# Kernel tuning notes

Measured on AMD Instinct MI355X. Metric: run time of the kernel, lower is better.

Reference implementation:

```python
import jax, jax.numpy as jnp
import numpy as np

HIDDEN = 2048
INTER = 768
N_EXPERTS = 64
TOP_K = 8
BATCH, SEQ = 2, 2048


def setup_inputs() -> dict:
    key = jax.random.key(0)
    k_x, k_g, k_gp, k_up, k_dp = jax.random.split(key, 5)
    s_in = 1.0 / np.sqrt(HIDDEN)   # lecun_normal fan_in scaling
    s_mid = 1.0 / np.sqrt(INTER)
    return {
        "x": jax.random.normal(k_x, (BATCH, SEQ, HIDDEN), dtype=jnp.float32),
        "gate_w": jax.random.normal(k_g, (HIDDEN, N_EXPERTS), dtype=jnp.float32) * s_in,
        "gate_proj": jax.random.normal(k_gp, (N_EXPERTS, HIDDEN, INTER), dtype=jnp.float32) * s_in,
        "up_proj": jax.random.normal(k_up, (N_EXPERTS, HIDDEN, INTER), dtype=jnp.float32) * s_in,
        "down_proj": jax.random.normal(k_dp, (N_EXPERTS, INTER, HIDDEN), dtype=jnp.float32) * s_mid,
    }


def reference(x, gate_w, gate_proj, up_proj, down_proj):
    H = x.shape[-1]
    E = gate_proj.shape[0]
    K = TOP_K

    x_flat = x.reshape(-1, H)                      # [T, H]
    router_logits = x_flat @ gate_w                # [T, E]

    routing_weights, selected_experts = jax.lax.top_k(router_logits, k=K)  # [T, K]
    routing_weights = jax.nn.softmax(routing_weights, axis=-1)

    sel_flat = jnp.ravel(selected_experts)         # [T*K]
    x_expanded = jnp.repeat(x_flat, K, axis=0)     # [T*K, H]

    sort_idx = jnp.argsort(sel_flat)
    unsort_idx = jnp.argsort(sort_idx)
    x_sorted = x_expanded[sort_idx]                # tokens grouped by expert
    group_sizes = jnp.bincount(sel_flat, length=E)

    gate_out = jax.lax.ragged_dot(x_sorted, gate_proj, group_sizes)  # [T*K, I]
    up_out = jax.lax.ragged_dot(x_sorted, up_proj, group_sizes)      # [T*K, I]
    activated = jax.nn.silu(gate_out) * up_out
    down_out = jax.lax.ragged_dot(activated, down_proj, group_sizes)  # [T*K, H]

    unsorted = down_out[unsort_idx].reshape(-1, K, H)  # [T, K, H]
    out = (unsorted * routing_weights[..., None]).sum(axis=1)
    return out.reshape(x.shape), router_logits
```

## Files before the change

kernel.cpp:

```cpp
#include <hip/hip_runtime.h>
#include <hip/hip_bf16.h>
#include <cstdint>

#define NTOK 4096
#define HID  2048
#define ITER 768
#define NEXP 64
#define TOPK 8
#define MAXT 320

typedef __attribute__((ext_vector_type(8))) short sh8;
typedef __attribute__((ext_vector_type(4))) float f32x4;

#define MFMA16 __builtin_amdgcn_mfma_f32_16x16x32_bf16

__device__ __forceinline__ uint16_t f2b(float f) {
  union { float f; uint32_t u; } v; v.f = f;
  uint32_t u = v.u;
  u += 0x7FFFu + ((u >> 16) & 1u);
  return (uint16_t)(u >> 16);
}

__device__ __forceinline__ float b2f_lo(uint32_t w) {
  union { uint32_t u; float f; } v; v.u = w << 16; return v.f;
}
__device__ __forceinline__ float b2f_hi(uint32_t w) {
  union { uint32_t u; float f; } v; v.u = w & 0xffff0000u; return v.f;
}

__device__ __forceinline__ uint32_t cvtpk(float lo, float hi) {
  float2 f2; f2.x = lo; f2.y = hi;
  __hip_bfloat162 h = __float22bfloat162_rn(f2);
  union { __hip_bfloat162 h; uint32_t u; } v; v.h = h;
  return v.u;
}

__device__ __forceinline__ void gl2lds16(const void* g, void* l) {
  __builtin_amdgcn_global_load_lds(
      (const __attribute__((address_space(1))) uint32_t*)g,
      (__attribute__((address_space(3))) uint32_t*)l, 16, 0, 0);
}

__device__ __forceinline__ int xcd_unswizzle(int s, int na) {
  int q = na >> 3, r = na & 7, x = s & 7, i = s >> 3;
  return (x < r ? x * (q + 1) : r * (q + 1) + (x - r) * q) + i;
}

__global__ void zero_kernel(int* __restrict__ cc) {
  cc[threadIdx.x] = 0;
}

__global__ __launch_bounds__(256) void xcast_kernel(const float* __restrict__ x,
                                                    uint16_t* __restrict__ xb) {
  size_t i = ((size_t)blockIdx.x * 256 + threadIdx.x) * 8;
  float4 a = *(const float4*)(x + i);
  float4 b = *(const float4*)(x + i + 4);
  uint4 o;
  o.x = (uint32_t)f2b(a.x) | ((uint32_t)f2b(a.y) << 16);
  o.y = (uint32_t)f2b(a.z) | ((uint32_t)f2b(a.w) << 16);
  o.z = (uint32_t)f2b(b.x) | ((uint32_t)f2b(b.y) << 16);
  o.w = (uint32_t)f2b(b.z) | ((uint32_t)f2b(b.w) << 16);
  *(uint4*)(xb + i) = o;
}

__global__ __launch_bounds__(256) void router_kernel(
    const float* __restrict__ x, const float* __restrict__ gate_w,
    float* __restrict__ logits, int* __restrict__ topk_id,
    float* __restrict__ topk_w, int* __restrict__ counts)
{
  int lane = threadIdx.x & 63;
  int wv   = threadIdx.x >> 6;
  int t    = blockIdx.x * 4 + wv;
  const float* xr = x + (size_t)t * HID;
  float acc = 0.f;
  #pragma unroll 4
  for (int h = 0; h < HID; h += 4) {
    float4 xv = *(const float4*)(xr + h);
    acc += xv.x * gate_w[(h + 0) * NEXP + lane];
    acc += xv.y * gate_w[(h + 1) * NEXP + lane];
    acc += xv.z * gate_w[(h + 2) * NEXP + lane];
    acc += xv.w * gate_w[(h + 3) * NEXP + lane];
  }
  logits[(size_t)t * NEXP + lane] = acc;

  float v = acc;
  float topv[TOPK]; int topi[TOPK];
  #pragma unroll
  for (int k = 0; k < TOPK; ++k) {
    float bv = v; int bi = lane;
    #pragma unroll
    for (int off = 32; off > 0; off >>= 1) {
      float ov = __shfl_xor(bv, off);
      int   oi = __shfl_xor(bi, off);
      if (ov > bv || (ov == bv && oi < bi)) { bv = ov; bi = oi; }
    }
    topv[k] = bv; topi[k] = bi;
    if (lane == bi) v = -3.0e38f;
  }
  float m = topv[0], s = 0.f, w[TOPK];
  #pragma unroll
  for (int k = 0; k < TOPK; ++k) { w[k] = __expf(topv[k] - m); s += w[k]; }
  float inv = 1.f / s;
  if (lane < TOPK) {
    topk_id[t * TOPK + lane] = topi[lane];
    topk_w[t * TOPK + lane]  = w[lane] * inv;
    atomicAdd(&counts[topi[lane]], 1);
  }
}

__global__ void offsets_kernel(const int* __restrict__ counts, int* __restrict__ offsets,
                               int* __restrict__ tiles, int* __restrict__ tilecount) {
  if (threadIdx.x == 0) {
    int s = 0, nt = 0;
    for (int e = 0; e < NEXP; ++e) {
      offsets[e] = s;
      int c = counts[e];
      for (int rb = 0; rb * 128 < c; ++rb) tiles[nt++] = (e << 16) | rb;
      s += c;
    }
    offsets[NEXP] = s;
    tilecount[0] = nt;
  }
}

__global__ __launch_bounds__(256) void scatter_kernel(
    const int* __restrict__ topk_id,
    const int* __restrict__ offsets, int* __restrict__ cursor,
    int* __restrict__ pair_tok, int* __restrict__ inv)
{
  int p = blockIdx.x * 256 + threadIdx.x;
  int e = topk_id[p];
  int pos = offsets[e] + atomicAdd(&cursor[e], 1);
  pair_tok[pos] = p;
  inv[p] = pos;
}

__global__ __launch_bounds__(256, 2) void gateup_kernel(
    const uint16_t* __restrict__ xb,
    const float* __restrict__ gate_proj,
    const float* __restrict__ up_proj,
    const int* __restrict__ pair_tok,
    const int* __restrict__ offsets,
    const int* __restrict__ tiles,
    const int* __restrict__ tilecount,
    uint16_t* __restrict__ act)
{
  const int nt = tilecount[0];
  const int na = nt * 12;
  if (blockIdx.x >= na) return;
  const int L  = xcd_unswizzle(blockIdx.x, na);
  const int ti = L % nt, nc = L / nt;
  const int te = tiles[ti];
  const int e = te >> 16, row0 = (te & 0xffff) * 128;
  const int start = offsets[e];
  const int count = offsets[e + 1] - start;
  const int nvalid = min(128, count - row0);

  __shared__ __align__(16) uint16_t aT[128 * 64];
  __shared__ __align__(16) uint16_t bT[128 * 64];
  __shared__ int s_tok[128];

  const int t = threadIdx.x, l = t & 63, w = t >> 6;
  if (t < 128)
    s_tok[t] = (t < nvalid) ? (pair_tok[start + row0 + t] >> 3) : 0;
  __syncthreads();

  const int sub = l >> 3;
  const int xk  = ((l & 7) ^ sub) << 3;
  const uint16_t* srcA[4]; char* dstA[4];
  #pragma unroll
  for (int q = 0; q < 4; ++q) {
    int rl = (w * 4 + q) * 8 + sub;
    srcA[q] = xb + (size_t)s_tok[rl] * HID + xk;
    dstA[q] = (char*)aT + (w * 4 + q) * 1024;
  }

  const int brow = t & 127;
  const int kk0  = (t >> 7) * 32;
  const int rcomb  = nc * 128 + brow;
  const int n_orig = ((rcomb >> 5) << 4) + (rcomb & 15);
  const int is_up  = (rcomb >> 4) & 1;
  const float* wsrc = (is_up ? up_proj : gate_proj)
                    + (size_t)e * HID * ITER + n_orig;
  uint16_t* bwr[4];
  #pragma unroll
  for (int s = 0; s < 4; ++s) {
    int kb = (kk0 * 2 + 16 * s) ^ ((brow & 7) << 4);
    bwr[s] = (uint16_t*)((char*)bT + brow * 128 + kb);
  }

  const int wr = w >> 1, wc = w & 1, lr = l & 15, hi = l >> 4;
  const int xorv = (lr & 7) << 4;

  f32x4 acc[4][4];
  #pragma unroll
  for (int mi = 0; mi < 4; ++mi)
    #pragma unroll
    for (int ni = 0; ni < 4; ++ni)
      acc[mi][ni] = (f32x4){0.f, 0.f, 0.f, 0.f};

  for (int kc = 0; kc < 32; ++kc) {
    __syncthreads();
    float va[32];
    const float* wp = wsrc + (size_t)(kc * 64 + kk0) * ITER;
    #pragma unroll
    for (int j = 0; j < 32; ++j) va[j] = wp[(size_t)j * ITER];
    #pragma unroll
    for (int q = 0; q < 4; ++q)
      gl2lds16(srcA[q] + kc * 64, dstA[q]);
    #pragma unroll
    for (int s = 0; s < 4; ++s) {
      uint4 o;
      o.x = cvtpk(va[s * 8 + 0], va[s * 8 + 1]);
      o.y = cvtpk(va[s * 8 + 2], va[s * 8 + 3]);
      o.z = cvtpk(va[s * 8 + 4], va[s * 8 + 5]);
      o.w = cvtpk(va[s * 8 + 6], va[s * 8 + 7]);
      *(uint4*)bwr[s] = o;
    }
    __syncthreads();
    #pragma unroll
    for (int ks = 0; ks < 2; ++ks) {
      sh8 af[4], bf[4];
      #pragma unroll
      for (int mi = 0; mi < 4; ++mi)
        af[mi] = *(const sh8*)((const char*)aT +
                   (wr * 64 + mi * 16 + lr) * 128 + ((ks * 64 + hi * 16) ^ xorv));
      #pragma unroll
      for (int ni = 0; ni < 4; ++ni)
        bf[ni] = *(const sh8*)((const char*)bT +
                   (wc * 64 + ni * 16 + lr) * 128 + ((ks * 64 + hi * 16) ^ xorv));
      #pragma unroll
      for (int mi = 0; mi < 4; ++mi)
        #pragma unroll
        for (int ni = 0; ni < 4; ++ni)
          acc[mi][ni] = MFMA16(af[mi], bf[ni], acc[mi][ni], 0, 0, 0);
    }
  }

  #pragma unroll
  for (int mi = 0; mi < 4; ++mi)
    #pragma unroll
    for (int p = 0; p < 2; ++p)
      #pragma unroll
      for (int j = 0; j < 4; ++j) {
        int row = wr * 64 + mi * 16 + hi * 4 + j;
        if (row < nvalid) {
          float g = acc[mi][2 * p][j], u = acc[mi][2 * p + 1][j];
          float a = (g / (1.f + __expf(-g))) * u;
          int col = nc * 64 + wc * 32 + p * 16 + lr;
          act[(size_t)(start + row0 + row) * ITER + col] = f2b(a);
        }
      }
}

__global__ __launch_bounds__(256, 2) void down_kernel(
    const uint16_t* __restrict__ act,
    const float* __restrict__ down_proj,
    const int* __restrict__ offsets,
    const int* __restrict__ tiles,
    const int* __restrict__ tilecount,
    uint16_t* __restrict__ dd)
{
  const int nt = tilecount[0];
  const int na = nt * 16;
  if (blockIdx.x >= na) return;
  const int L  = xcd_unswizzle(blockIdx.x, na);
  const int ti = L % nt, nc = L / nt;
  const int te = tiles[ti];
  const int e = te >> 16, row0 = (te & 0xffff) * 128;
  const int start = offsets[e];
  const int count = offsets[e + 1] - start;
  const int nvalid = min(128, count - row0);

  __shared__ __align__(16) uint16_t aT[128 * 64];
  __shared__ __align__(16) uint16_t bT[128 * 64];

  const int t = threadIdx.x, l = t & 63, w = t >> 6;

  const int sub = l >> 3;
  const int xk  = ((l & 7) ^ sub) << 3;

  const uint16_t* srcA[4]; char* dstA[4];
  #pragma unroll
  for (int q = 0; q < 4; ++q) {
    int rl = (w * 4 + q) * 8 + sub;
    srcA[q] = act + (size_t)(start + row0 + rl) * ITER + xk;
    dstA[q] = (char*)aT + (w * 4 + q) * 1024;
  }

  const int brow = t & 127;
  const int kk0  = (t >> 7) * 32;
  const float* wsrc = down_proj + (size_t)e * ITER * HID + nc * 128 + brow;
  uint16_t* bwr[4];
  #pragma unroll
  for (int s = 0; s < 4; ++s) {
    int kb = (kk0 * 2 + 16 * s) ^ ((brow & 7) << 4);
    bwr[s] = (uint16_t*)((char*)bT + brow * 128 + kb);
  }

  const int wr = w >> 1, wc = w & 1, lr = l & 15, hi = l >> 4;
  const int xorv = (lr & 7) << 4;

  f32x4 acc[4][4];
  #pragma unroll
  for (int mi = 0; mi < 4; ++mi)
    #pragma unroll
    for (int ni = 0; ni < 4; ++ni)
      acc[mi][ni] = (f32x4){0.f, 0.f, 0.f, 0.f};

  for (int kc = 0; kc < 12; ++kc) {
    __syncthreads();
    float va[32];
    const float* wp = wsrc + (size_t)(kc * 64 + kk0) * HID;
    #pragma unroll
    for (int j = 0; j < 32; ++j) va[j] = wp[(size_t)j * HID];
    #pragma unroll
    for (int q = 0; q < 4; ++q)
      gl2lds16(srcA[q] + kc * 64, dstA[q]);
    #pragma unroll
    for (int s = 0; s < 4; ++s) {
      uint4 o;
      o.x = cvtpk(va[s * 8 + 0], va[s * 8 + 1]);
      o.y = cvtpk(va[s * 8 + 2], va[s * 8 + 3]);
      o.z = cvtpk(va[s * 8 + 4], va[s * 8 + 5]);
      o.w = cvtpk(va[s * 8 + 6], va[s * 8 + 7]);
      *(uint4*)bwr[s] = o;
    }
    __syncthreads();
    #pragma unroll
    for (int ks = 0; ks < 2; ++ks) {
      sh8 af[4], bf[4];
      #pragma unroll
      for (int mi = 0; mi < 4; ++mi)
        af[mi] = *(const sh8*)((const char*)aT +
                   (wr * 64 + mi * 16 + lr) * 128 + ((ks * 64 + hi * 16) ^ xorv));
      #pragma unroll
      for (int ni = 0; ni < 4; ++ni)
        bf[ni] = *(const sh8*)((const char*)bT +
                   (wc * 64 + ni * 16 + lr) * 128 + ((ks * 64 + hi * 16) ^ xorv));
      #pragma unroll
      for (int mi = 0; mi < 4; ++mi)
        #pragma unroll
        for (int ni = 0; ni < 4; ++ni)
          acc[mi][ni] = MFMA16(af[mi], bf[ni], acc[mi][ni], 0, 0, 0);
    }
  }

  #pragma unroll
  for (int mi = 0; mi < 4; ++mi)
    #pragma unroll
    for (int ni = 0; ni < 4; ++ni)
      #pragma unroll
      for (int j = 0; j < 4; ++j) {
        int row = wr * 64 + mi * 16 + hi * 4 + j;
        if (row < nvalid) {
          int col = nc * 128 + wc * 64 + ni * 16 + lr;
          dd[(size_t)(start + row0 + row) * HID + col] = f2b(acc[mi][ni][j]);
        }
      }
}

__global__ __launch_bounds__(256) void reduce_kernel(
    const uint16_t* __restrict__ dd, const float* __restrict__ topk_w,
    const int* __restrict__ inv, float* __restrict__ out)
{
  const int tok = blockIdx.x;
  const int c   = threadIdx.x * 8;
  float acc[8] = {0.f, 0.f, 0.f, 0.f, 0.f, 0.f, 0.f, 0.f};
  #pragma unroll
  for (int k = 0; k < TOPK; ++k) {
    const int   pos = inv[tok * TOPK + k];
    const float wk  = topk_w[tok * TOPK + k];
    uint4 v = *(const uint4*)&dd[(size_t)pos * HID + c];
    acc[0] += wk * b2f_lo(v.x);  acc[1] += wk * b2f_hi(v.x);
    acc[2] += wk * b2f_lo(v.y);  acc[3] += wk * b2f_hi(v.y);
    acc[4] += wk * b2f_lo(v.z);  acc[5] += wk * b2f_hi(v.z);
    acc[6] += wk * b2f_lo(v.w);  acc[7] += wk * b2f_hi(v.w);
  }
  float4 o0 = {acc[0], acc[1], acc[2], acc[3]};
  float4 o1 = {acc[4], acc[5], acc[6], acc[7]};
  float* op = out + (size_t)tok * HID + c;
  *(float4*)op       = o0;
  *(float4*)(op + 4) = o1;
}

extern "C" void kernel_launch(void* const* d_in, const int* in_sizes, int n_in,
                              void* d_out, int out_size, void* d_ws, size_t ws_size,
                              hipStream_t stream) {
  const float* x         = (const float*)d_in[0];
  const float* gate_w    = (const float*)d_in[1];
  const float* gate_proj = (const float*)d_in[2];
  const float* up_proj   = (const float*)d_in[3];
  const float* down_proj = (const float*)d_in[4];

  float* out    = (float*)d_out;
  float* logits = out + (size_t)NTOK * HID;

  char* ws = (char*)d_ws;
  size_t off = 0;
  uint16_t* xb      = (uint16_t*)(ws + off); off += (size_t)NTOK * HID * 2;
  uint16_t* act     = (uint16_t*)(ws + off); off += (size_t)(NTOK * TOPK + 128) * ITER * 2;
  uint16_t* dd      = (uint16_t*)(ws + off); off += (size_t)(NTOK * TOPK + 128) * HID * 2;
  int*      topk_id = (int*)  (ws + off); off += (size_t)NTOK * TOPK * 4;
  float*    topk_w  = (float*)(ws + off); off += (size_t)NTOK * TOPK * 4;
  int*      counts  = (int*)  (ws + off); off += 256;
  int*      cursor  = (int*)  (ws + off); off += 256;
  int*      offsets = (int*)  (ws + off); off += 512;
  int*      tiles   = (int*)  (ws + off); off += MAXT * 4;
  int*      tilecount=(int*)  (ws + off); off += 256;
  int*      pair_tok= (int*)  (ws + off); off += (size_t)NTOK * TOPK * 4;
  int*      inv     = (int*)  (ws + off); off += (size_t)NTOK * TOPK * 4;

  zero_kernel   <<<1,    128, 0, stream>>>(counts);
  xcast_kernel  <<<4096, 256, 0, stream>>>(x, xb);
  router_kernel <<<1024, 256, 0, stream>>>(x, gate_w, logits, topk_id, topk_w, counts);
  offsets_kernel<<<1,    64,  0, stream>>>(counts, offsets, tiles, tilecount);
  scatter_kernel<<<128,  256, 0, stream>>>(topk_id, offsets, cursor, pair_tok, inv);

  gateup_kernel<<<MAXT * 12, 256, 0, stream>>>(xb, gate_proj, up_proj, pair_tok, offsets,
                                               tiles, tilecount, act);
  down_kernel  <<<MAXT * 16, 256, 0, stream>>>(act, down_proj, offsets,
                                               tiles, tilecount, dd);
  reduce_kernel<<<NTOK, 256, 0, stream>>>(dd, topk_w, inv, out);
}
```

Before: 940.9 us.

## Halve N tile to 64 and prefetch next weight chunk into registers during MFMA

Both grouped GEMM kernels shrink the per-block output width from 128 to 64 columns, doubling the grid and raising the launch-bounds occupancy hint from 2 to 4 blocks per CU. The fp32 weight loads for the next K chunk are now issued into registers before the MFMA loop of the current chunk, so global latency overlaps compute. The cost is that each token tile's A data is reloaded twice as often, giving more activation traffic and a lower MFMA-to-load ratio per block.

Result: slower. 1.073 ms (+14.1%).

```diff
diff --git a/kernel.cpp b/kernel.cpp
--- a/kernel.cpp
+++ b/kernel.cpp
@@ -135,7 +135,7 @@
   inv[p] = pos;
 }
 
-__global__ __launch_bounds__(256, 2) void gateup_kernel(
+__global__ __launch_bounds__(256, 4) void gateup_kernel(
     const uint16_t* __restrict__ xb,
     const float* __restrict__ gate_proj,
     const float* __restrict__ up_proj,
@@ -146,7 +146,7 @@
     uint16_t* __restrict__ act)
 {
   const int nt = tilecount[0];
-  const int na = nt * 12;
+  const int na = nt * 24;
   if (blockIdx.x >= na) return;
   const int L  = xcd_unswizzle(blockIdx.x, na);
   const int ti = L % nt, nc = L / nt;
@@ -157,7 +157,7 @@
   const int nvalid = min(128, count - row0);
 
   __shared__ __align__(16) uint16_t aT[128 * 64];
-  __shared__ __align__(16) uint16_t bT[128 * 64];
+  __shared__ __align__(16) uint16_t bT[64 * 64];
   __shared__ int s_tok[128];
 
   const int t = threadIdx.x, l = t & 63, w = t >> 6;
@@ -175,16 +175,16 @@
     dstA[q] = (char*)aT + (w * 4 + q) * 1024;
   }
 
-  const int brow = t & 127;
-  const int kk0  = (t >> 7) * 32;
-  const int rcomb  = nc * 128 + brow;
+  const int brow = t & 63;
+  const int kk0  = (t >> 6) * 16;
+  const int rcomb  = nc * 64 + brow;
   const int n_orig = ((rcomb >> 5) << 4) + (rcomb & 15);
   const int is_up  = (rcomb >> 4) & 1;
   const float* wsrc = (is_up ? up_proj : gate_proj)
                     + (size_t)e * HID * ITER + n_orig;
-  uint16_t* bwr[4];
-  #pragma unroll
-  for (int s = 0; s < 4; ++s) {
+  uint16_t* bwr[2];
+  #pragma unroll
+  for (int s = 0; s < 2; ++s) {
     int kb = (kk0 * 2 + 16 * s) ^ ((brow & 7) << 4);
     bwr[s] = (uint16_t*)((char*)bT + brow * 128 + kb);
   }
@@ -192,47 +192,55 @@
   const int wr = w >> 1, wc = w & 1, lr = l & 15, hi = l >> 4;
   const int xorv = (lr & 7) << 4;
 
-  f32x4 acc[4][4];
+  f32x4 acc[4][2];
   #pragma unroll
   for (int mi = 0; mi < 4; ++mi)
     #pragma unroll
-    for (int ni = 0; ni < 4; ++ni)
+    for (int ni = 0; ni < 2; ++ni)
       acc[mi][ni] = (f32x4){0.f, 0.f, 0.f, 0.f};
+
+  float va[16];
+  {
+    const float* wp = wsrc + (size_t)kk0 * ITER;
+    #pragma unroll
+    for (int j = 0; j < 16; ++j) va[j] = wp[(size_t)j * ITER];
+  }
 
   for (int kc = 0; kc < 32; ++kc) {
     __syncthreads();
-    float va[32];
-    const float* wp = wsrc + (size_t)(kc * 64 + kk0) * ITER;
-    #pragma unroll
-    for (int j = 0; j < 32; ++j) va[j] = wp[(size_t)j * ITER];
+    {
+      uint4 o0, o1;
+      o0.x = cvtpk(va[0],  va[1]);  o0.y = cvtpk(va[2],  va[3]);
+      o0.z = cvtpk(va[4],  va[5]);  o0.w = cvtpk(va[6],  va[7]);
+      o1.x = cvtpk(va[8],  va[9]);  o1.y = cvtpk(va[10], va[11]);
+      o1.z = cvtpk(va[12], va[13]); o1.w = cvtpk(va[14], va[15]);
+      *(uint4*)bwr[0] = o0;
+      *(uint4*)bwr[1] = o1;
+    }
     #pragma unroll
     for (int q = 0; q < 4; ++q)
       gl2lds16(srcA[q] + kc * 64, dstA[q]);
-    #pragma unroll
-    for (int s = 0; s < 4; ++s) {
-      uint4 o;
-      o.x = cvtpk(va[s * 8 + 0], va[s * 8 + 1]);
-      o.y = cvtpk(va[s * 8 + 2], va[s * 8 + 3]);
-      o.z = cvtpk(va[s * 8 + 4], va[s * 8 + 5]);
-      o.w = cvtpk(va[s * 8 + 6], va[s * 8 + 7]);
-      *(uint4*)bwr[s] = o;
-    }
     __syncthreads();
+    if (kc + 1 < 32) {
+      const float* wp = wsrc + (size_t)((kc + 1) * 64 + kk0) * ITER;
+      #pragma unroll
+      for (int j = 0; j < 16; ++j) va[j] = wp[(size_t)j * ITER];
+    }
     #pragma unroll
     for (int ks = 0; ks < 2; ++ks) {
-      sh8 af[4], bf[4];
+      sh8 af[4], bf[2];
       #pragma unroll
       for (int mi = 0; mi < 4; ++mi)
         af[mi] = *(const sh8*)((const char*)aT +
                    (wr * 64 + mi * 16 + lr) * 128 + ((ks * 64 + hi * 16) ^ xorv));
       #pragma unroll
-      for (int ni = 0; ni < 4; ++ni)
+      for (int ni = 0; ni < 2; ++ni)
         bf[ni] = *(const sh8*)((const char*)bT +
-                   (wc * 64 + ni * 16 + lr) * 128 + ((ks * 64 + hi * 16) ^ xorv));
+                   (wc * 32 + ni * 16 + lr) * 128 + ((ks * 64 + hi * 16) ^ xorv));
       #pragma unroll
       for (int mi = 0; mi < 4; ++mi)
         #pragma unroll
-        for (int ni = 0; ni < 4; ++ni)
+        for (int ni = 0; ni < 2; ++ni)
           acc[mi][ni] = MFMA16(af[mi], bf[ni], acc[mi][ni], 0, 0, 0);
     }
   }
@@ -240,20 +248,18 @@
   #pragma unroll
   for (int mi = 0; mi < 4; ++mi)
     #pragma unroll
-    for (int p = 0; p < 2; ++p)
-      #pragma unroll
-      for (int j = 0; j < 4; ++j) {
-        int row = wr * 64 + mi * 16 + hi * 4 + j;
-        if (row < nvalid) {
-          float g = acc[mi][2 * p][j], u = acc[mi][2 * p + 1][j];
-          float a = (g / (1.f + __expf(-g))) * u;
-          int col = nc * 64 + wc * 32 + p * 16 + lr;
-          act[(size_t)(start + row0 + row) * ITER + col] = f2b(a);
-        }
+    for (int j = 0; j < 4; ++j) {
+      int row = wr * 64 + mi * 16 + hi * 4 + j;
+      if (row < nvalid) {
+        float g = acc[mi][0][j], u = acc[mi][1][j];
+        float a = (g / (1.f + __expf(-g))) * u;
+        int col = (nc * 2 + wc) * 16 + lr;
+        act[(size_t)(start + row0 + row) * ITER + col] = f2b(a);
       }
-}
-
-__global__ __launch_bounds__(256, 2) void down_kernel(
+    }
+}
+
+__global__ __launch_bounds__(256, 4) void down_kernel(
     const uint16_t* __restrict__ act,
     const float* __restrict__ down_proj,
     const int* __restrict__ offsets,
@@ -262,7 +268,7 @@
     uint16_t* __restrict__ dd)
 {
   const int nt = tilecount[0];
-  const int na = nt * 16;
+  const int na = nt * 32;
   if (blockIdx.x >= na) return;
   const int L  = xcd_unswizzle(blockIdx.x, na);
   const int ti = L % nt, nc = L / nt;
@@ -273,7 +279,7 @@
   const int nvalid = min(128, count - row0);
 
   __shared__ __align__(16) uint16_t aT[128 * 64];
-  __shared__ __align__(16) uint16_t bT[128 * 64];
+  __shared__ __align__(16) uint16_t bT[64 * 64];
 
   const int t = threadIdx.x, l = t & 63, w = t >> 6;
 
@@ -288,12 +294,12 @@
     dstA[q] = (char*)aT + (w * 4 + q) * 1024;
   }
 
-  const int brow = t & 127;
-  const int kk0  = (t >> 7) * 32;
-  const float* wsrc = down_proj + (size_t)e * ITER * HID + nc * 128 + brow;
-  uint16_t* bwr[4];
-  #pragma unroll
-  for (int s = 0; s < 4; ++s) {
+  const int brow = t & 63;
+  const int kk0  = (t >> 6) * 16;
+  const float* wsrc = down_proj + (size_t)e * ITER * HID + nc * 64 + brow;
+  uint16_t* bwr[2];
+  #pragma unroll
+  for (int s = 0; s < 2; ++s) {
     int kb = (kk0 * 2 + 16 * s) ^ ((brow & 7) << 4);
     bwr[s] = (uint16_t*)((char*)bT + brow * 128 + kb);
   }
@@ -301,47 +307,55 @@
   const int wr = w >> 1, wc = w & 1, lr = l & 15, hi = l >> 4;
   const int xorv = (lr & 7) << 4;
 
-  f32x4 acc[4][4];
+  f32x4 acc[4][2];
   #pragma unroll
   for (int mi = 0; mi < 4; ++mi)
     #pragma unroll
-    for (int ni = 0; ni < 4; ++ni)
+    for (int ni = 0; ni < 2; ++ni)
       acc[mi][ni] = (f32x4){0.f, 0.f, 0.f, 0.f};
+
+  float va[16];
+  {
+    const float* wp = wsrc + (size_t)kk0 * HID;
+    #pragma unroll
+    for (int j = 0; j < 16; ++j) va[j] = wp[(size_t)j * HID];
+  }
 
   for (int kc = 0; kc < 12; ++kc) {
     __syncthreads();
-    float va[32];
-    const float* wp = wsrc + (size_t)(kc * 64 + kk0) * HID;
-    #pragma unroll
-    for (int j = 0; j < 32; ++j) va[j] = wp[(size_t)j * HID];
+    {
+      uint4 o0, o1;
+      o0.x = cvtpk(va[0],  va[1]);  o0.y = cvtpk(va[2],  va[3]);
+      o0.z = cvtpk(va[4],  va[5]);  o0.w = cvtpk(va[6],  va[7]);
+      o1.x = cvtpk(va[8],  va[9]);  o1.y = cvtpk(va[10], va[11]);
+      o1.z = cvtpk(va[12], va[13]); o1.w = cvtpk(va[14], va[15]);
+      *(uint4*)bwr[0] = o0;
+      *(uint4*)bwr[1] = o1;
+    }
     #pragma unroll
     for (int q = 0; q < 4; ++q)
       gl2lds16(srcA[q] + kc * 64, dstA[q]);
-    #pragma unroll
-    for (int s = 0; s < 4; ++s) {
-      uint4 o;
-      o.x = cvtpk(va[s * 8 + 0], va[s * 8 + 1]);
-      o.y = cvtpk(va[s * 8 + 2], va[s * 8 + 3]);
-      o.z = cvtpk(va[s * 8 + 4], va[s * 8 + 5]);
-      o.w = cvtpk(va[s * 8 + 6], va[s * 8 + 7]);
-      *(uint4*)bwr[s] = o;
-    }
     __syncthreads();
+    if (kc + 1 < 12) {
+      const float* wp = wsrc + (size_t)((kc + 1) * 64 + kk0) * HID;
+      #pragma unroll
+      for (int j = 0; j < 16; ++j) va[j] = wp[(size_t)j * HID];
+    }
     #pragma unroll
     for (int ks = 0; ks < 2; ++ks) {
-      sh8 af[4], bf[4];
+      sh8 af[4], bf[2];
       #pragma unroll
       for (int mi = 0; mi < 4; ++mi)
         af[mi] = *(const sh8*)((const char*)aT +
                    (wr * 64 + mi * 16 + lr) * 128 + ((ks * 64 + hi * 16) ^ xorv));
       #pragma unroll
-      for (int ni = 0; ni < 4; ++ni)
+      for (int ni = 0; ni < 2; ++ni)
         bf[ni] = *(const sh8*)((const char*)bT +
-                   (wc * 64 + ni * 16 + lr) * 128 + ((ks * 64 + hi * 16) ^ xorv));
+                   (wc * 32 + ni * 16 + lr) * 128 + ((ks * 64 + hi * 16) ^ xorv));
       #pragma unroll
       for (int mi = 0; mi < 4; ++mi)
         #pragma unroll
-        for (int ni = 0; ni < 4; ++ni)
+        for (int ni = 0; ni < 2; ++ni)
           acc[mi][ni] = MFMA16(af[mi], bf[ni], acc[mi][ni], 0, 0, 0);
     }
   }
@@ -349,12 +363,12 @@
   #pragma unroll
   for (int mi = 0; mi < 4; ++mi)
     #pragma unroll
-    for (int ni = 0; ni < 4; ++ni)
+    for (int ni = 0; ni < 2; ++ni)
       #pragma unroll
       for (int j = 0; j < 4; ++j) {
         int row = wr * 64 + mi * 16 + hi * 4 + j;
         if (row < nvalid) {
-          int col = nc * 128 + wc * 64 + ni * 16 + lr;
+          int col = nc * 64 + wc * 32 + ni * 16 + lr;
           dd[(size_t)(start + row0 + row) * HID + col] = f2b(acc[mi][ni][j]);
         }
       }
@@ -417,9 +431,9 @@
   offsets_kernel<<<1,    64,  0, stream>>>(counts, offsets, tiles, tilecount);
   scatter_kernel<<<128,  256, 0, stream>>>(topk_id, offsets, cursor, pair_tok, inv);
 
-  gateup_kernel<<<MAXT * 12, 256, 0, stream>>>(xb, gate_proj, up_proj, pair_tok, offsets,
+  gateup_kernel<<<MAXT * 24, 256, 0, stream>>>(xb, gate_proj, up_proj, pair_tok, offsets,
                                                tiles, tilecount, act);
-  down_kernel  <<<MAXT * 16, 256, 0, stream>>>(act, down_proj, offsets,
+  down_kernel  <<<MAXT * 32, 256, 0, stream>>>(act, down_proj, offsets,
                                                tiles, tilecount, dd);
   reduce_kernel<<<NTOK, 256, 0, stream>>>(dd, topk_w, inv, out);
 }
```
